# Optimization experiments

Hardware: AMD Instinct MI355X
Metric: run time of the kernel (lower is better)

Reference implementation:

```python
import jax, jax.numpy as jnp
from jax import lax
import numpy as np

B, C_IN, D, H, W = 1, 8, 48, 256, 320
BC = 8  # base_channels
DN = ('NCHW', 'OIHW', 'NCHW')


def setup_inputs() -> dict:
    key = jax.random.key(0)
    ks = iter(jax.random.split(key, 64))
    inp = {"volume_variance": jax.random.normal(next(ks), (B, C_IN, D, H, W), jnp.float32)}
    def add(name, o, i):
        inp[name + "_w"] = jax.random.normal(next(ks), (o, i, 3, 3), jnp.float32) * 0.1
        inp[name + "_b"] = jnp.zeros((o,), jnp.float32)
    add("conv1", 2 * BC, C_IN); add("conv2", 4 * BC, 2 * BC); add("conv3", 8 * BC, 4 * BC)
    add("up3", 4 * BC, 8 * BC); add("up2", 2 * BC, 4 * BC); add("up1", BC, 2 * BC)
    add("out", 1, BC)
    add("g1_gate", 2 * BC, C_IN + BC); add("g1_cand", BC, C_IN + BC)
    add("g2_gate", 4 * BC, 4 * BC); add("g2_cand", 2 * BC, 4 * BC)
    add("g3_gate", 8 * BC, 8 * BC); add("g3_cand", 4 * BC, 8 * BC)
    add("g4_gate", 16 * BC, 16 * BC); add("g4_cand", 8 * BC, 16 * BC)
    return inp


def _conv(x, w, b, stride=1):
    # Conv2d(k=3, padding=1)
    y = lax.conv_general_dilated(x, w, (stride, stride), [(1, 1), (1, 1)], dimension_numbers=DN)
    return y + b[None, :, None, None]


def _convT(x, w, b):
    # PyTorch ConvTranspose2d(k=3, s=2, p=1, output_padding=1) as an input-dilated conv
    y = lax.conv_general_dilated(x, w, (1, 1), [(1, 2), (1, 2)], lhs_dilation=(2, 2),
                                 dimension_numbers=DN)
    return y + b[None, :, None, None]


def _gru(x, h, wg, bg, wc, bc):
    # ConvGRUCell2: fused reset/update gates, tanh candidate, convex combine
    gates = jax.nn.sigmoid(_conv(jnp.concatenate([x, h], 1), wg, bg))
    r, u = jnp.split(gates, 2, 1)
    c = jnp.tanh(_conv(jnp.concatenate([x, r * h], 1), wc, bc))
    return u * h + (1.0 - u) * c


def reference(volume_variance, conv1_w, conv1_b, conv2_w, conv2_b, conv3_w, conv3_b,
              up3_w, up3_b, up2_w, up2_b, up1_w, up1_b, out_w, out_b,
              g1_gate_w, g1_gate_b, g1_cand_w, g1_cand_b,
              g2_gate_w, g2_gate_b, g2_cand_w, g2_cand_b,
              g3_gate_w, g3_gate_b, g3_cand_w, g3_cand_b,
              g4_gate_w, g4_gate_b, g4_cand_w, g4_cand_b):
    def step(carry, cost):
        s1, s2, s3, s4 = carry
        nc = -cost                                            # [B, C_IN, H, W]
        c1 = jax.nn.relu(_conv(nc, conv1_w, conv1_b, 2))      # [B, 2BC, H/2, W/2]
        c2 = jax.nn.relu(_conv(c1, conv2_w, conv2_b, 2))      # [B, 4BC, H/4, W/4]
        c3 = jax.nn.relu(_conv(c2, conv3_w, conv3_b, 2))      # [B, 8BC, H/8, W/8]
        r4 = _gru(c3, s4, g4_gate_w, g4_gate_b, g4_cand_w, g4_cand_b)
        u3 = jax.nn.relu(_convT(r4, up3_w, up3_b))            # [B, 4BC, H/4, W/4]
        r3 = _gru(c2, s3, g3_gate_w, g3_gate_b, g3_cand_w, g3_cand_b)
        u2 = jax.nn.relu(_convT(u3 + r3, up2_w, up2_b))       # [B, 2BC, H/2, W/2]
        r2 = _gru(c1, s2, g2_gate_w, g2_gate_b, g2_cand_w, g2_cand_b)
        u1 = jax.nn.relu(_convT(u2 + r2, up1_w, up1_b))       # [B, BC, H, W]
        r1 = _gru(nc, s1, g1_gate_w, g1_gate_b, g1_cand_w, g1_cand_b)
        # ConvTranspose2d(k=3, s=1, p=1, op=0) is exactly a 3x3 same-pad conv (reparam'd weight)
        reg = _conv(u1 + r1, out_w, out_b)                    # [B, 1, H, W]
        return (r1, r2, r3, r4), reg[:, 0]
    costs = jnp.moveaxis(volume_variance, 2, 0)               # [D, B, C_IN, H, W]
    init = (jnp.zeros((B, BC, H, W), jnp.float32),
            jnp.zeros((B, 2 * BC, H // 2, W // 2), jnp.float32),
            jnp.zeros((B, 4 * BC, H // 4, W // 4), jnp.float32),
            jnp.zeros((B, 8 * BC, H // 8, W // 8), jnp.float32))
    _, outs = lax.scan(step, init, costs)                     # outs: [D, B, H, W]
    return jnp.moveaxis(outs, 0, 1)                           # [B, D, H, W]
```

## Files before the change

### kernel.cpp

```cpp
#include <hip/hip_runtime.h>
#include <math.h>

namespace {

constexpr int H0 = 256, W0 = 320, H1 = 128, W1 = 160, H2 = 64, W2 = 80, H3 = 32, W3 = 40;
constexpr int HW0 = H0 * W0, HW1 = H1 * W1, HW2 = H2 * W2, HW3 = H3 * W3;
constexpr int DEPTH = 48;
constexpr int NCS = DEPTH * HW0;

__device__ __forceinline__ int xcd_remap(int b, int n) {
  const int q = n >> 3, r = n & 7, xcd = b & 7, i = b >> 3;
  return (xcd < r ? xcd * (q + 1) : r * (q + 1) + (xcd - r) * q) + i;
}

template <int CX, int CH, int COUT, int QX, int QY, int OCPT, int CHUNK,
          bool NEGX, bool CAND, int ZC, bool UNIF>
__device__ __forceinline__ void gru_conv_q(
    int bx, int by, int zg, int H, int W,
    const float* __restrict__ x, int xcs,
    const float* __restrict__ h, const float* __restrict__ rg,
    const float* __restrict__ wT, const float* __restrict__ bias,
    float* __restrict__ out, float* lds) {
  constexpr int CIN = CX + CH, TPX = 2 * QX, TPY = 2 * QY;
  constexpr int IW = TPX + 2, IH = TPY + 2;
  constexpr int NQ = QX * QY, SUBS = 256 / NQ;
  static_assert(SUBS * OCPT * ZC == COUT, "cfg");
  static_assert(CHUNK * IH * IW <= 6400, "lds");
  const int x0 = bx * TPX, y0 = by * TPY, HW = H * W, tid = threadIdx.x;
  const int q = tid % NQ, sub = tid / NQ;
  const int qx = q % QX, qy = q / QX;
  int ocb = zg * (COUT / ZC) + sub * OCPT;
  if (UNIF) ocb = __builtin_amdgcn_readfirstlane(ocb);
  float acc[OCPT][4];
#pragma unroll
  for (int j = 0; j < OCPT; j++) {
    const float bb = bias[ocb + j];
    acc[j][0] = bb; acc[j][1] = bb; acc[j][2] = bb; acc[j][3] = bb;
  }
  for (int c0 = 0; c0 < CIN; c0 += CHUNK) {
    __syncthreads();
    for (int idx = tid; idx < CHUNK * IH * IW; idx += 256) {
      const int cc = idx / (IH * IW), rr = idx % (IH * IW), yy = rr / IW, xx = rr % IW;
      const int gy = y0 + yy - 1, gx = x0 + xx - 1, c = c0 + cc;
      float v = 0.f;
      if ((unsigned)gy < (unsigned)H && (unsigned)gx < (unsigned)W) {
        if (c < CX) {
          v = x[(size_t)c * xcs + gy * W + gx];
          if (NEGX) v = -v;
        } else {
          const int p = (c - CX) * HW + gy * W + gx;
          v = h[p];
          if (CAND) v *= rg[p];
        }
      }
      lds[idx] = v;
    }
    __syncthreads();
    for (int c = 0; c < CHUNK; c++) {
      float p[4][4];
      const float* lp = lds + (c * IH + 2 * qy) * IW + 2 * qx;
#pragma unroll
      for (int r = 0; r < 4; r++) {
        const float2 a = *(const float2*)(lp + r * IW);
        const float2 b = *(const float2*)(lp + r * IW + 2);
        p[r][0] = a.x; p[r][1] = a.y; p[r][2] = b.x; p[r][3] = b.y;
      }
#pragma unroll
      for (int j = 0; j < OCPT; j++) {
        const float* wc = wT + ((size_t)(c0 + c) * COUT + ocb + j) * 9;
#pragma unroll
        for (int ky = 0; ky < 3; ky++)
#pragma unroll
          for (int kx = 0; kx < 3; kx++) {
            const float wv = wc[ky * 3 + kx];
            acc[j][0] = fmaf(p[ky][kx],         wv, acc[j][0]);
            acc[j][1] = fmaf(p[ky][kx + 1],     wv, acc[j][1]);
            acc[j][2] = fmaf(p[ky + 1][kx],     wv, acc[j][2]);
            acc[j][3] = fmaf(p[ky + 1][kx + 1], wv, acc[j][3]);
          }
      }
    }
  }
  const int ox = x0 + 2 * qx, oy = y0 + 2 * qy;
#pragma unroll
  for (int j = 0; j < OCPT; j++) {
    const int oc = ocb + j;
#pragma unroll
    for (int py = 0; py < 2; py++)
#pragma unroll
      for (int px = 0; px < 2; px++) {
        const int opix = (oy + py) * W + ox + px;
        const float a = acc[j][py * 2 + px];
        if (!CAND) {
          out[oc * HW + opix] = 1.f / (1.f + expf(-a));
        } else {
          const float cd = tanhf(a);
          const float u = rg[(CH + oc) * HW + opix];
          const float hv = h[oc * HW + opix];
          out[oc * HW + opix] = u * hv + (1.f - u) * cd;
        }
      }
  }
}

struct GruArgs {
  const float* x;
  const float* c1; const float* c2; const float* c3;
  const float* h1; const float* h2; const float* h3; const float* h4;
  const float* g1; const float* g2; const float* g3; const float* g4;
  const float* w1; const float* b1; const float* w2; const float* b2;
  const float* w3; const float* b3; const float* w4; const float* b4;
  float* o1; float* o2; float* o3; float* o4;
};

__global__ __launch_bounds__(256) void gates_k(GruArgs a) {
  __shared__ __align__(16) float lds[6400];
  const int b = xcd_remap(blockIdx.x, 1120);
  if (b < 320) {
    gru_conv_q<8, 8, 16, 8, 8, 4, 16, true, false, 1, true>(
        b % 20, b / 20, 0, H0, W0, a.x, NCS, a.h1, nullptr, a.w1, a.b1, a.o1, lds);
  } else if (b < 640) {
    const int l = b - 320;
    gru_conv_q<16, 16, 32, 8, 8, 2, 16, false, false, 4, true>(
        l % 10, (l / 10) % 8, l / 80, H1, W1, a.c1, HW1, a.h2, nullptr, a.w2, a.b2, a.o2, lds);
  } else if (b < 960) {
    const int l = b - 640;
    gru_conv_q<32, 32, 64, 4, 4, 1, 32, false, false, 4, false>(
        l % 10, (l / 10) % 8, l / 80, H2, W2, a.c2, HW2, a.h3, nullptr, a.w3, a.b3, a.o3, lds);
  } else {
    const int l = b - 960;
    gru_conv_q<64, 64, 128, 4, 4, 1, 64, false, false, 8, false>(
        l % 5, (l / 5) % 4, l / 20, H3, W3, a.c3, HW3, a.h4, nullptr, a.w4, a.b4, a.o4, lds);
  }
}

__global__ __launch_bounds__(256) void cands_k(GruArgs a) {
  __shared__ __align__(16) float lds[6400];
  const int b = xcd_remap(blockIdx.x, 720);
  if (b < 320) {
    gru_conv_q<8, 8, 8, 8, 8, 2, 16, true, true, 1, true>(
        b % 20, b / 20, 0, H0, W0, a.x, NCS, a.h1, a.g1, a.w1, a.b1, a.o1, lds);
  } else if (b < 480) {
    const int l = b - 320;
    gru_conv_q<16, 16, 16, 8, 8, 2, 16, false, true, 2, true>(
        l % 10, (l / 10) % 8, l / 80, H1, W1, a.c1, HW1, a.h2, a.g2, a.w2, a.b2, a.o2, lds);
  } else if (b < 640) {
    const int l = b - 480;
    gru_conv_q<32, 32, 32, 4, 4, 1, 32, false, true, 2, false>(
        l % 10, (l / 10) % 8, l / 80, H2, W2, a.c2, HW2, a.h3, a.g3, a.w3, a.b3, a.o3, lds);
  } else {
    const int l = b - 640;
    gru_conv_q<64, 64, 64, 4, 4, 1, 64, false, true, 4, false>(
        l % 5, (l / 5) % 4, l / 20, H3, W3, a.c3, HW3, a.h4, a.g4, a.w4, a.b4, a.o4, lds);
  }
}

template <int CIN, int COUT, int QX, int QY, int OCPT, int CHUNK, bool NEG,
          int INH, int INW, int ONH, int ONW, bool UNIF>
__global__ __launch_bounds__(256) void enc_q_k(
    const float* __restrict__ in, int inCS, size_t inTS, int inSlots,
    const float* __restrict__ wT, const float* __restrict__ bias,
    float* __restrict__ out, size_t outTS, int outSlots, int t0, int n) {
  constexpr int TPX = 2 * QX, TPY = 2 * QY, IW = 2 * TPX + 1, IH = 2 * TPY + 1;
  constexpr int SX = ONW / TPX, SY = ONH / TPY, NQ = QX * QY, SUBS = 256 / NQ;
  static_assert(SUBS * OCPT == COUT, "cfg");
  __shared__ float lds[CHUNK * IH * IW];
  const int lb = xcd_remap(blockIdx.x, n);
  const int z = lb / (SX * SY), rr = lb % (SX * SY);
  const int bx = rr % SX, by = rr / SX, tt = t0 + z;
  const float* inp = in + (size_t)(tt % inSlots) * inTS;
  float* outp = out + (size_t)(tt % outSlots) * outTS;
  const int x0 = bx * TPX, y0 = by * TPY;
  const int ix0 = 2 * x0 - 1, iy0 = 2 * y0 - 1, tid = threadIdx.x;
  const int q = tid % NQ, sub = tid / NQ, qx = q % QX, qy = q / QX;
  int ocb = sub * OCPT;
  if (UNIF) ocb = __builtin_amdgcn_readfirstlane(ocb);
  float acc[OCPT][4];
#pragma unroll
  for (int j = 0; j < OCPT; j++) {
    const float bb = bias[ocb + j];
    acc[j][0] = bb; acc[j][1] = bb; acc[j][2] = bb; acc[j][3] = bb;
  }
  for (int c0 = 0; c0 < CIN; c0 += CHUNK) {
    __syncthreads();
    for (int idx = tid; idx < CHUNK * IH * IW; idx += 256) {
      const int cc = idx / (IH * IW), r2 = idx % (IH * IW), yy = r2 / IW, xx = r2 % IW;
      const int gy = iy0 + yy, gx = ix0 + xx;
      float v = 0.f;
      if ((unsigned)gy < (unsigned)INH && (unsigned)gx < (unsigned)INW)
        v = inp[(size_t)(c0 + cc) * inCS + gy * INW + gx];
      lds[idx] = NEG ? -v : v;
    }
    __syncthreads();
    for (int c = 0; c < CHUNK; c++) {
      float p[5][5];
      const float* lp = lds + (c * IH + 4 * qy) * IW + 4 * qx;
#pragma unroll
      for (int r = 0; r < 5; r++)
#pragma unroll
        for (int s = 0; s < 5; s++) p[r][s] = lp[r * IW + s];
#pragma unroll
      for (int j = 0; j < OCPT; j++) {
        const float* wc = wT + ((size_t)(c0 + c) * COUT + ocb + j) * 9;
#pragma unroll
        for (int ky = 0; ky < 3; ky++)
#pragma unroll
          for (int kx = 0; kx < 3; kx++) {
            const float wv = wc[ky * 3 + kx];
            acc[j][0] = fmaf(p[ky][kx],         wv, acc[j][0]);
            acc[j][1] = fmaf(p[ky][kx + 2],     wv, acc[j][1]);
            acc[j][2] = fmaf(p[ky + 2][kx],     wv, acc[j][2]);
            acc[j][3] = fmaf(p[ky + 2][kx + 2], wv, acc[j][3]);
          }
      }
    }
  }
  const int ox = x0 + 2 * qx, oy = y0 + 2 * qy;
#pragma unroll
  for (int j = 0; j < OCPT; j++)
#pragma unroll
    for (int py = 0; py < 2; py++)
#pragma unroll
      for (int px = 0; px < 2; px++)
        outp[((size_t)(ocb + j) * ONH + oy + py) * ONW + ox + px] =
            fmaxf(acc[j][py * 2 + px], 0.f);
}

template <int CIN, int COUT, int OCPT, bool SUM2, int INH, int INW>
__global__ __launch_bounds__(256) void convT_q_k(
    const float* __restrict__ A, size_t aTS, int aSlots,
    const float* __restrict__ B, size_t bTS, int bSlots,
    const float* __restrict__ wT, const float* __restrict__ bias,
    float* __restrict__ out, size_t oTS, int oSlots, int t0, int n) {
  constexpr int SX = (2 * INW) / 16, SY = (2 * INH) / 16, SUBS = 16;
  static_assert(SUBS * OCPT == COUT, "cfg");
  __shared__ float lds[CIN * 81];
  const int lb = xcd_remap(blockIdx.x, n);
  const int z = lb / (SX * SY), rr = lb % (SX * SY);
  const int bx = rr % SX, by = rr / SX, tt = t0 + z;
  const float* Ap = A + (size_t)(tt % aSlots) * aTS;
  const float* Bp = B + (size_t)(tt % bSlots) * bTS;
  float* outp = out + (size_t)(tt % oSlots) * oTS;
  const int x0 = bx * 16, y0 = by * 16, ix0 = x0 / 2, iy0 = y0 / 2;
  const int HWin = INH * INW, tid = threadIdx.x;
  for (int idx = tid; idx < CIN * 81; idx += 256) {
    const int c = idx / 81, r = idx % 81, yy = r / 9, xx = r % 9;
    const int gy = iy0 + yy, gx = ix0 + xx;
    float v = 0.f;
    if (gy < INH && gx < INW) {
      const int p = c * HWin + gy * INW + gx;
      v = Ap[p];
      if (SUM2) v += Bp[p];
    }
    lds[idx] = v;
  }
  __syncthreads();
  const int cb = tid % 16, sub = tid / 16;
  const int cbx = cb % 4, cby = cb / 4;
  const int ocb = sub * OCPT;
  float a00[OCPT][4], a01[OCPT][4], a10[OCPT][4], a11[OCPT][4];
#pragma unroll
  for (int j = 0; j < OCPT; j++) {
    const float bb = bias[ocb + j];
#pragma unroll
    for (int qi = 0; qi < 4; qi++) {
      a00[j][qi] = bb; a01[j][qi] = bb; a10[j][qi] = bb; a11[j][qi] = bb;
    }
  }
  for (int c = 0; c < CIN; c++) {
    float p[3][3];
    const float* ip = lds + c * 81 + (2 * cby) * 9 + 2 * cbx;
#pragma unroll
    for (int r = 0; r < 3; r++)
#pragma unroll
      for (int s = 0; s < 3; s++) p[r][s] = ip[r * 9 + s];
#pragma unroll
    for (int j = 0; j < OCPT; j++) {
      const float* wc = wT + ((size_t)c * COUT + ocb + j) * 9;
      const float w0 = wc[0], w1 = wc[1], w2 = wc[2], w3 = wc[3], w4 = wc[4];
      const float w5 = wc[5], w6 = wc[6], w7 = wc[7], w8 = wc[8];
#pragma unroll
      for (int dy = 0; dy < 2; dy++)
#pragma unroll
        for (int dx = 0; dx < 2; dx++) {
          const int qi = dy * 2 + dx;
          const float v00 = p[dy][dx], v01 = p[dy][dx + 1];
          const float v10 = p[dy + 1][dx], v11 = p[dy + 1][dx + 1];
          a00[j][qi] = fmaf(w4, v00, a00[j][qi]);
          a01[j][qi] = fmaf(w3, v00, a01[j][qi]);
          a01[j][qi] = fmaf(w5, v01, a01[j][qi]);
          a10[j][qi] = fmaf(w1, v00, a10[j][qi]);
          a10[j][qi] = fmaf(w7, v10, a10[j][qi]);
          a11[j][qi] = fmaf(w0, v00, a11[j][qi]);
          a11[j][qi] = fmaf(w2, v01, a11[j][qi]);
          a11[j][qi] = fmaf(w6, v10, a11[j][qi]);
          a11[j][qi] = fmaf(w8, v11, a11[j][qi]);
        }
    }
  }
  const int outW = 2 * INW;
#pragma unroll
  for (int j = 0; j < OCPT; j++) {
    float* op = outp + (size_t)(ocb + j) * (4 * HWin);
#pragma unroll
    for (int dy = 0; dy < 2; dy++)
#pragma unroll
      for (int dx = 0; dx < 2; dx++) {
        const int qi = dy * 2 + dx;
        const int ox = x0 + 2 * (2 * cbx + dx), oy = y0 + 2 * (2 * cby + dy);
        const int base = oy * outW + ox;
        op[base] = fmaxf(a00[j][qi], 0.f);
        op[base + 1] = fmaxf(a01[j][qi], 0.f);
        op[base + outW] = fmaxf(a10[j][qi], 0.f);
        op[base + outW + 1] = fmaxf(a11[j][qi], 0.f);
      }
  }
}

__global__ __launch_bounds__(256) void up1out_k(
    const float* __restrict__ u2, size_t u2TS, int u2S,
    const float* __restrict__ r2, size_t r2TS, int r2S,
    const float* __restrict__ r1, size_t r1TS, int r1S,
    const float* __restrict__ wTu1, const float* __restrict__ bT,
    const float* __restrict__ wo, const float* __restrict__ bo,
    float* __restrict__ dout, int t0, int n) {
  __shared__ float ins[16 * 121];
  __shared__ float u1h[8 * 400];
  const int lb = xcd_remap(blockIdx.x, n);
  const int z = lb / 320, rr = lb % 320, bx = rr % 20, by = rr / 20;
  const int t = t0 + z;
  const float* U = u2 + (size_t)(t % u2S) * u2TS;
  const float* R2 = r2 + (size_t)(t % r2S) * r2TS;
  const float* R1 = r1 + (size_t)(t % r1S) * r1TS;
  const int x0 = bx * 16, y0 = by * 16;
  const int ix0 = x0 / 2 - 1, iy0 = y0 / 2 - 1, tid = threadIdx.x;
  for (int idx = tid; idx < 16 * 121; idx += 256) {
    const int c = idx / 121, r = idx % 121, yy = r / 11, xx = r % 11;
    const int gy = iy0 + yy, gx = ix0 + xx;
    float v = 0.f;
    if ((unsigned)gy < (unsigned)H1 && (unsigned)gx < (unsigned)W1) {
      const int p = c * HW1 + gy * W1 + gx;
      v = U[p] + R2[p];
    }
    ins[idx] = v;
  }
  __syncthreads();
  if (tid < 200) {
    const int ch = tid / 25, cb = tid % 25, cbx = cb % 5, cby = cb / 5;
    const float bb = bT[ch];
    float A0[4], A1[4], A2[4], A3[4];
#pragma unroll
    for (int qi = 0; qi < 4; qi++) { A0[qi] = bb; A1[qi] = bb; A2[qi] = bb; A3[qi] = bb; }
    for (int ic = 0; ic < 16; ic++) {
      float p[3][3];
      const float* ip = ins + ic * 121 + (2 * cby) * 11 + 2 * cbx;
#pragma unroll
      for (int r = 0; r < 3; r++)
#pragma unroll
        for (int s = 0; s < 3; s++) p[r][s] = ip[r * 11 + s];
      const float* wc = wTu1 + ((size_t)ic * 8 + ch) * 9;
      const float w0 = wc[0], w1 = wc[1], w2 = wc[2], w3 = wc[3], w4 = wc[4];
      const float w5 = wc[5], w6 = wc[6], w7 = wc[7], w8 = wc[8];
#pragma unroll
      for (int dy = 0; dy < 2; dy++)
#pragma unroll
        for (int dx = 0; dx < 2; dx++) {
          const int qi = dy * 2 + dx;
          const float v00 = p[dy][dx], v01 = p[dy][dx + 1];
          const float v10 = p[dy + 1][dx], v11 = p[dy + 1][dx + 1];
          A0[qi] = fmaf(w4, v00, A0[qi]);
          A1[qi] = fmaf(w3, v00, A1[qi]); A1[qi] = fmaf(w5, v01, A1[qi]);
          A2[qi] = fmaf(w1, v00, A2[qi]); A2[qi] = fmaf(w7, v10, A2[qi]);
          A3[qi] = fmaf(w0, v00, A3[qi]); A3[qi] = fmaf(w2, v01, A3[qi]);
          A3[qi] = fmaf(w6, v10, A3[qi]); A3[qi] = fmaf(w8, v11, A3[qi]);
        }
    }
#pragma unroll
    for (int dy = 0; dy < 2; dy++)
#pragma unroll
      for (int dx = 0; dx < 2; dx++) {
        const int qi = dy * 2 + dx;
        float* up = u1h + ch * 400 + (2 * (2 * cby + dy)) * 20 + 2 * (2 * cbx + dx);
        up[0] = fmaxf(A0[qi], 0.f);
        up[1] = fmaxf(A1[qi], 0.f);
        up[20] = fmaxf(A2[qi], 0.f);
        up[21] = fmaxf(A3[qi], 0.f);
      }
  }
  __syncthreads();
  for (int idx = tid; idx < 8 * 400; idx += 256) {
    const int c = idx / 400, r = idx % 400, hy = r / 20, hx = r % 20;
    const int gy = y0 - 2 + hy, gx = x0 - 2 + hx;
    if ((unsigned)gy < (unsigned)H0 && (unsigned)gx < (unsigned)W0)
      u1h[idx] += R1[c * HW0 + gy * W0 + gx];
    else
      u1h[idx] = 0.f;
  }
  __syncthreads();
  const int tx = tid % 16, ty = tid / 16;
  float acc = bo[0];
  for (int c = 0; c < 8; c++) {
    const float* up = u1h + c * 400 + (ty + 1) * 20 + tx + 1;
#pragma unroll
    for (int ky = 0; ky < 3; ky++)
#pragma unroll
      for (int kx = 0; kx < 3; kx++)
        acc = fmaf(up[ky * 20 + kx], wo[c * 9 + ky * 3 + kx], acc);
  }
  dout[(size_t)t * HW0 + (y0 + ty) * W0 + x0 + tx] = acc;
}

struct WT { const float* s; float* d; int O; int I; };
struct WTab { WT t[14]; };
__global__ __launch_bounds__(256) void wtrans_k(WTab a) {
  for (int ti = 0; ti < 14; ti++) {
    const int O = a.t[ti].O, I = a.t[ti].I, nn = O * I * 9;
    for (int idx = blockIdx.x * 256 + threadIdx.x; idx < nn; idx += gridDim.x * 256) {
      const int k = idx % 9, oi = idx / 9;
      const int i = oi % I, o = oi / I;
      a.t[ti].d[((size_t)i * O + o) * 9 + k] = a.t[ti].s[idx];
    }
  }
}

}

extern "C" void kernel_launch(void* const* d_in, const int* in_sizes, int n_in,
                              void* d_out, int out_size, void* d_ws, size_t ws_size,
                              hipStream_t stream) {
  const float* vol = (const float*)d_in[0];
  const float* c1w = (const float*)d_in[1];  const float* c1b = (const float*)d_in[2];
  const float* c2w = (const float*)d_in[3];  const float* c2b = (const float*)d_in[4];
  const float* c3w = (const float*)d_in[5];  const float* c3b = (const float*)d_in[6];
  const float* u3w = (const float*)d_in[7];  const float* u3b = (const float*)d_in[8];
  const float* u2w = (const float*)d_in[9];  const float* u2b = (const float*)d_in[10];
  const float* u1w = (const float*)d_in[11]; const float* u1b = (const float*)d_in[12];
  const float* ow  = (const float*)d_in[13]; const float* ob  = (const float*)d_in[14];
  const float* g1gw = (const float*)d_in[15]; const float* g1gb = (const float*)d_in[16];
  const float* g1cw = (const float*)d_in[17]; const float* g1cb = (const float*)d_in[18];
  const float* g2gw = (const float*)d_in[19]; const float* g2gb = (const float*)d_in[20];
  const float* g2cw = (const float*)d_in[21]; const float* g2cb = (const float*)d_in[22];
  const float* g3gw = (const float*)d_in[23]; const float* g3gb = (const float*)d_in[24];
  const float* g3cw = (const float*)d_in[25]; const float* g3cb = (const float*)d_in[26];
  const float* g4gw = (const float*)d_in[27]; const float* g4gb = (const float*)d_in[28];
  const float* g4cw = (const float*)d_in[29]; const float* g4cb = (const float*)d_in[30];
  float* dout = (float*)d_out;
  (void)in_sizes; (void)n_in; (void)out_size;

  const size_t r1Sz = 8 * HW0, r2Sz = 16 * HW1, r3Sz = 32 * HW2, r4Sz = 64 * HW3;
  const size_t c1Sz = 16 * HW1, c2Sz = 32 * HW2, c3Sz = 64 * HW3;
  const size_t g1Sz = 16 * HW0, g2Sz = 32 * HW1, g3Sz = 64 * HW2, g4Sz = 128 * HW3;
  const size_t ZB = 8 * HW0;
  const size_t rTot = r1Sz + r2Sz + r3Sz + r4Sz;
  const size_t cTot = c1Sz + c2Sz + c3Sz;
  const size_t gTot = g1Sz + g2Sz + g3Sz + g4Sz;
  const size_t uTot = 32 * HW2 + 16 * HW1;
  const size_t wTot = 342144;
  const size_t needA = (wTot + ZB + 48 * rTot + 48 * cTot + gTot) * sizeof(float);
  const size_t needB = (wTot + ZB + 2 * rTot + 48 * cTot + gTot + uTot) * sizeof(float);
  const int tier = ws_size >= needA ? 0 : (ws_size >= needB ? 1 : 2);
  const int TR = (tier == 0) ? 48 : 2;
  const int TC = (tier == 2) ? 1 : 48;

  float* ws = (float*)d_ws;
  size_t off = 0;
  auto alloc = [&](size_t nn) { float* p = ws + off; off += nn; return p; };
  float* wt_c1 = alloc(1152);   float* wt_c2 = alloc(4608);  float* wt_c3 = alloc(18432);
  float* wt_u3 = alloc(18432);  float* wt_u2 = alloc(4608);  float* wt_u1 = alloc(1152);
  float* wt_g1g = alloc(2304);  float* wt_g1c = alloc(1152);
  float* wt_g2g = alloc(9216);  float* wt_g2c = alloc(4608);
  float* wt_g3g = alloc(36864); float* wt_g3c = alloc(18432);
  float* wt_g4g = alloc(147456); float* wt_g4c = alloc(73728);
  float* zb = alloc(ZB);
  float* r1 = alloc((size_t)TR * r1Sz); float* r2 = alloc((size_t)TR * r2Sz);
  float* r3 = alloc((size_t)TR * r3Sz); float* r4 = alloc((size_t)TR * r4Sz);
  float* g1 = alloc(g1Sz); float* g2 = alloc(g2Sz);
  float* g3 = alloc(g3Sz); float* g4 = alloc(g4Sz);
  float* c1a = alloc((size_t)TC * c1Sz);
  float* c2a = alloc((size_t)TC * c2Sz);
  float* c3a = alloc((size_t)TC * c3Sz);
  float *u3a, *u2a;
  if (tier == 0) {
    u3a = c1a;
    u2a = c1a + 48 * (32 * HW2);
  } else {
    u3a = alloc(32 * HW2);
    u2a = alloc(16 * HW1);
  }

  WTab wt{{{c1w, wt_c1, 16, 8},   {c2w, wt_c2, 32, 16},  {c3w, wt_c3, 64, 32},
           {u3w, wt_u3, 32, 64},  {u2w, wt_u2, 16, 32},  {u1w, wt_u1, 8, 16},
           {g1gw, wt_g1g, 16, 16}, {g1cw, wt_g1c, 8, 16},
           {g2gw, wt_g2g, 32, 32}, {g2cw, wt_g2c, 16, 32},
           {g3gw, wt_g3g, 64, 64}, {g3cw, wt_g3c, 32, 64},
           {g4gw, wt_g4g, 128, 128}, {g4cw, wt_g4c, 64, 128}}};
  wtrans_k<<<dim3(128), 256, 0, stream>>>(wt);
  hipMemsetAsync(zb, 0, ZB * sizeof(float), stream);

  if (tier < 2) {
    enc_q_k<8, 16, 8, 8, 4, 8, true, 256, 320, 128, 160, true>
        <<<dim3(3840), 256, 0, stream>>>(vol, NCS, (size_t)HW0, 48, wt_c1, c1b,
                                         c1a, c1Sz, 48, 0, 3840);
    enc_q_k<16, 32, 8, 8, 8, 8, false, 128, 160, 64, 80, true>
        <<<dim3(960), 256, 0, stream>>>(c1a, HW1, c1Sz, 48, wt_c2, c2b,
                                        c2a, c2Sz, 48, 0, 960);
    enc_q_k<32, 64, 4, 4, 4, 16, false, 64, 80, 32, 40, false>
        <<<dim3(960), 256, 0, stream>>>(c2a, HW2, c2Sz, 48, wt_c3, c3b,
                                        c3a, c3Sz, 48, 0, 960);
  }

  for (int t = 0; t < DEPTH; t++) {
    if (tier == 2) {
      enc_q_k<8, 16, 8, 8, 4, 8, true, 256, 320, 128, 160, true>
          <<<dim3(80), 256, 0, stream>>>(vol, NCS, (size_t)HW0, 48, wt_c1, c1b,
                                         c1a, c1Sz, 1, t, 80);
      enc_q_k<16, 32, 8, 8, 8, 8, false, 128, 160, 64, 80, true>
          <<<dim3(20), 256, 0, stream>>>(c1a, HW1, c1Sz, 1, wt_c2, c2b,
                                         c2a, c2Sz, 1, t, 20);
      enc_q_k<32, 64, 4, 4, 4, 16, false, 64, 80, 32, 40, false>
          <<<dim3(20), 256, 0, stream>>>(c2a, HW2, c2Sz, 1, wt_c3, c3b,
                                         c3a, c3Sz, 1, t, 20);
    }
    const float* x0p = vol + (size_t)t * HW0;
    const float* h1p = t ? r1 + (size_t)((t - 1) % TR) * r1Sz : zb;
    const float* h2p = t ? r2 + (size_t)((t - 1) % TR) * r2Sz : zb;
    const float* h3p = t ? r3 + (size_t)((t - 1) % TR) * r3Sz : zb;
    const float* h4p = t ? r4 + (size_t)((t - 1) % TR) * r4Sz : zb;
    const float* c1p = c1a + (size_t)(t % TC) * c1Sz;
    const float* c2p = c2a + (size_t)(t % TC) * c2Sz;
    const float* c3p = c3a + (size_t)(t % TC) * c3Sz;
    float* o1p = r1 + (size_t)(t % TR) * r1Sz;
    float* o2p = r2 + (size_t)(t % TR) * r2Sz;
    float* o3p = r3 + (size_t)(t % TR) * r3Sz;
    float* o4p = r4 + (size_t)(t % TR) * r4Sz;

    GruArgs ga{x0p, c1p, c2p, c3p, h1p, h2p, h3p, h4p,
               nullptr, nullptr, nullptr, nullptr,
               wt_g1g, g1gb, wt_g2g, g2gb, wt_g3g, g3gb, wt_g4g, g4gb,
               g1, g2, g3, g4};
    gates_k<<<dim3(1120), 256, 0, stream>>>(ga);
    GruArgs ca{x0p, c1p, c2p, c3p, h1p, h2p, h3p, h4p,
               g1, g2, g3, g4,
               wt_g1c, g1cb, wt_g2c, g2cb, wt_g3c, g3cb, wt_g4c, g4cb,
               o1p, o2p, o3p, o4p};
    cands_k<<<dim3(720), 256, 0, stream>>>(ca);

    if (tier > 0) {
      convT_q_k<64, 32, 2, false, 32, 40>
          <<<dim3(20), 256, 0, stream>>>(r4, r4Sz, TR, r4, 0, 1, wt_u3, u3b,
                                         u3a, (size_t)32 * HW2, 1, t, 20);
      convT_q_k<32, 16, 1, true, 64, 80>
          <<<dim3(80), 256, 0, stream>>>(u3a, (size_t)32 * HW2, 1, r3, r3Sz, TR,
                                         wt_u2, u2b, u2a, (size_t)16 * HW1, 1, t, 80);
      up1out_k<<<dim3(320), 256, 0, stream>>>(
          u2a, (size_t)16 * HW1, 1, r2, r2Sz, TR, r1, r1Sz, TR,
          wt_u1, u1b, ow, ob, dout, t, 320);
    }
  }

  if (tier == 0) {
    convT_q_k<64, 32, 2, false, 32, 40>
        <<<dim3(960), 256, 0, stream>>>(r4, r4Sz, 48, r4, 0, 1, wt_u3, u3b,
                                        u3a, (size_t)32 * HW2, 48, 0, 960);
    convT_q_k<32, 16, 1, true, 64, 80>
        <<<dim3(3840), 256, 0, stream>>>(u3a, (size_t)32 * HW2, 48, r3, r3Sz, 48,
                                         wt_u2, u2b, u2a, (size_t)16 * HW1, 48, 0, 3840);
    up1out_k<<<dim3(15360), 256, 0, stream>>>(
        u2a, (size_t)16 * HW1, 48, r2, r2Sz, 48, r1, r1Sz, 48,
        wt_u1, u1b, ow, ob, dout, 0, 15360);
  }
}
```

Measured before the change: 9.838 ms.

## Restructure GRU conv tiling to one pixel per thread with wave-uniform channels

Replaces the 2x2-quad-per-thread GRU conv with a one-output-pixel-per-thread scheme. The level-1 path uses 16x16 tiles with all output channels per thread, and the coarser levels use 8x8 tiles with a per-wave channel group read via readfirstlane. Multi-chunk levels precompute packed gather offsets once and load larger channel chunks into LDS. Launch bounds now request 5 blocks per CU, grids are rebalanced, and the final up1out launch in tier 0 is split into four smaller launches. Together this trades quad-level input reuse for scalar weight broadcasts and higher occupancy, with more register pressure from the wide per-thread channel accumulators.

```diff
diff --git a/kernel.cpp b/kernel.cpp
--- a/kernel.cpp
+++ b/kernel.cpp
@@ -13,42 +13,58 @@
   return (xcd < r ? xcd * (q + 1) : r * (q + 1) + (xcd - r) * q) + i;
 }
 
-template <int CX, int CH, int COUT, int QX, int QY, int OCPT, int CHUNK,
-          bool NEGX, bool CAND, int ZC, bool UNIF>
-__device__ __forceinline__ void gru_conv_q(
+template <int CX, int CH, int COUT, int TW, int TH, int OCW, int CHUNK,
+          bool AMODE, bool NEGX, bool CAND>
+__device__ __forceinline__ void gru5(
     int bx, int by, int zg, int H, int W,
     const float* __restrict__ x, int xcs,
     const float* __restrict__ h, const float* __restrict__ rg,
     const float* __restrict__ wT, const float* __restrict__ bias,
     float* __restrict__ out, float* lds) {
-  constexpr int CIN = CX + CH, TPX = 2 * QX, TPY = 2 * QY;
-  constexpr int IW = TPX + 2, IH = TPY + 2;
-  constexpr int NQ = QX * QY, SUBS = 256 / NQ;
-  static_assert(SUBS * OCPT * ZC == COUT, "cfg");
-  static_assert(CHUNK * IH * IW <= 6400, "lds");
-  const int x0 = bx * TPX, y0 = by * TPY, HW = H * W, tid = threadIdx.x;
-  const int q = tid % NQ, sub = tid / NQ;
-  const int qx = q % QX, qy = q / QX;
-  int ocb = zg * (COUT / ZC) + sub * OCPT;
-  if (UNIF) ocb = __builtin_amdgcn_readfirstlane(ocb);
-  float acc[OCPT][4];
-#pragma unroll
-  for (int j = 0; j < OCPT; j++) {
-    const float bb = bias[ocb + j];
-    acc[j][0] = bb; acc[j][1] = bb; acc[j][2] = bb; acc[j][3] = bb;
-  }
-  for (int c0 = 0; c0 < CIN; c0 += CHUNK) {
-    __syncthreads();
-    for (int idx = tid; idx < CHUNK * IH * IW; idx += 256) {
-      const int cc = idx / (IH * IW), rr = idx % (IH * IW), yy = rr / IW, xx = rr % IW;
-      const int gy = y0 + yy - 1, gx = x0 + xx - 1, c = c0 + cc;
+  constexpr int CIN = CX + CH, IW = TW + 2, IH = TH + 2, NST = IH * IW;
+  constexpr int NCHK = CIN / CHUNK, TOTAL = CHUNK * NST;
+  static_assert(NCHK * CHUNK == CIN, "chunk");
+  static_assert(AMODE ? (TW == 16 && TH == 16) : (TW == 8 && TH == 8), "tile");
+  const int tid = threadIdx.x, wv = tid >> 6, ln = tid & 63;
+  const int x0 = bx * TW, y0 = by * TH, HW = H * W;
+  int lx, ly, ocb;
+  if (AMODE) {
+    lx = ln & 15; ly = (wv << 2) + (ln >> 4); ocb = 0;
+  } else {
+    lx = ln & 7; ly = ln >> 3;
+    ocb = __builtin_amdgcn_readfirstlane((zg * 4 + wv) * OCW);
+  }
+  float acc[OCW];
+#pragma unroll
+  for (int j = 0; j < OCW; j++) acc[j] = bias[ocb + j];
+
+  auto compute = [&](int c0) {
+    for (int c = 0; c < CHUNK; c++) {
+      float v[9];
+      const float* lp = lds + (c * IH + ly) * IW + lx;
+#pragma unroll
+      for (int ky = 0; ky < 3; ky++)
+#pragma unroll
+        for (int kx = 0; kx < 3; kx++) v[ky * 3 + kx] = lp[ky * IW + kx];
+      const float* wb = wT + ((size_t)(c0 + c) * COUT + ocb) * 9;
+#pragma unroll
+      for (int j = 0; j < OCW; j++)
+#pragma unroll
+        for (int k = 0; k < 9; k++) acc[j] = fmaf(v[k], wb[j * 9 + k], acc[j]);
+    }
+  };
+
+  if constexpr (NCHK == 1) {
+    for (int idx = tid; idx < TOTAL; idx += 256) {
+      const int cc = idx / NST, rr = idx % NST, yy = rr / IW, xx = rr % IW;
+      const int gy = y0 + yy - 1, gx = x0 + xx - 1;
       float v = 0.f;
       if ((unsigned)gy < (unsigned)H && (unsigned)gx < (unsigned)W) {
-        if (c < CX) {
-          v = x[(size_t)c * xcs + gy * W + gx];
+        if (cc < CX) {
+          v = x[(size_t)cc * xcs + gy * W + gx];
           if (NEGX) v = -v;
         } else {
-          const int p = (c - CX) * HW + gy * W + gx;
+          const int p = (cc - CX) * HW + gy * W + gx;
           v = h[p];
           if (CAND) v *= rg[p];
         }
@@ -56,50 +72,57 @@
       lds[idx] = v;
     }
     __syncthreads();
-    for (int c = 0; c < CHUNK; c++) {
-      float p[4][4];
-      const float* lp = lds + (c * IH + 2 * qy) * IW + 2 * qx;
-#pragma unroll
-      for (int r = 0; r < 4; r++) {
-        const float2 a = *(const float2*)(lp + r * IW);
-        const float2 b = *(const float2*)(lp + r * IW + 2);
-        p[r][0] = a.x; p[r][1] = a.y; p[r][2] = b.x; p[r][3] = b.y;
+    compute(0);
+  } else {
+    constexpr int NIT = TOTAL / 256;
+    static_assert(NIT * 256 == TOTAL, "items");
+    unsigned pk[NIT];
+#pragma unroll
+    for (int i = 0; i < NIT; i++) {
+      const int idx = tid + 256 * i;
+      const int cc = idx / NST, rr = idx % NST, yy = rr / IW, xx = rr % IW;
+      const int gy = y0 + yy - 1, gx = x0 + xx - 1;
+      const bool val = (unsigned)gy < (unsigned)H && (unsigned)gx < (unsigned)W;
+      const unsigned ro = val ? (unsigned)(gy * W + gx) : 0u;
+      pk[i] = (val ? 0x80000000u : 0u) | ((unsigned)cc << 20) | ro;
+    }
+    for (int c0 = 0; c0 < CIN; c0 += CHUNK) {
+      if (c0) __syncthreads();
+#pragma unroll
+      for (int i = 0; i < NIT; i++) {
+        const unsigned u = pk[i];
+        float v = 0.f;
+        if (u & 0x80000000u) {
+          const int c = c0 + (int)((u >> 20) & 0x3ffu);
+          const int ro = (int)(u & 0xfffffu);
+          if (c < CX) {
+            v = x[(size_t)c * xcs + ro];
+            if (NEGX) v = -v;
+          } else {
+            const int p = (c - CX) * HW + ro;
+            v = h[p];
+            if (CAND) v *= rg[p];
+          }
+        }
+        lds[tid + 256 * i] = v;
       }
-#pragma unroll
-      for (int j = 0; j < OCPT; j++) {
-        const float* wc = wT + ((size_t)(c0 + c) * COUT + ocb + j) * 9;
-#pragma unroll
-        for (int ky = 0; ky < 3; ky++)
-#pragma unroll
-          for (int kx = 0; kx < 3; kx++) {
-            const float wv = wc[ky * 3 + kx];
-            acc[j][0] = fmaf(p[ky][kx],         wv, acc[j][0]);
-            acc[j][1] = fmaf(p[ky][kx + 1],     wv, acc[j][1]);
-            acc[j][2] = fmaf(p[ky + 1][kx],     wv, acc[j][2]);
-            acc[j][3] = fmaf(p[ky + 1][kx + 1], wv, acc[j][3]);
-          }
-      }
-    }
-  }
-  const int ox = x0 + 2 * qx, oy = y0 + 2 * qy;
-#pragma unroll
-  for (int j = 0; j < OCPT; j++) {
+      __syncthreads();
+      compute(c0);
+    }
+  }
+
+  const int opix = (y0 + ly) * W + x0 + lx;
+#pragma unroll
+  for (int j = 0; j < OCW; j++) {
     const int oc = ocb + j;
-#pragma unroll
-    for (int py = 0; py < 2; py++)
-#pragma unroll
-      for (int px = 0; px < 2; px++) {
-        const int opix = (oy + py) * W + ox + px;
-        const float a = acc[j][py * 2 + px];
-        if (!CAND) {
-          out[oc * HW + opix] = 1.f / (1.f + expf(-a));
-        } else {
-          const float cd = tanhf(a);
-          const float u = rg[(CH + oc) * HW + opix];
-          const float hv = h[oc * HW + opix];
-          out[oc * HW + opix] = u * hv + (1.f - u) * cd;
-        }
-      }
+    if (!CAND) {
+      out[oc * HW + opix] = 1.f / (1.f + expf(-acc[j]));
+    } else {
+      const float cd = tanhf(acc[j]);
+      const float u = rg[(CH + oc) * HW + opix];
+      const float hv = h[oc * HW + opix];
+      out[oc * HW + opix] = u * hv + (1.f - u) * cd;
+    }
   }
 }
 
@@ -113,45 +136,45 @@
   float* o1; float* o2; float* o3; float* o4;
 };
 
-__global__ __launch_bounds__(256) void gates_k(GruArgs a) {
+__global__ __launch_bounds__(256, 5) void gates_k(GruArgs a) {
   __shared__ __align__(16) float lds[6400];
-  const int b = xcd_remap(blockIdx.x, 1120);
+  const int b = xcd_remap(blockIdx.x, 1280);
   if (b < 320) {
-    gru_conv_q<8, 8, 16, 8, 8, 4, 16, true, false, 1, true>(
+    gru5<8, 8, 16, 16, 16, 16, 16, true, true, false>(
         b % 20, b / 20, 0, H0, W0, a.x, NCS, a.h1, nullptr, a.w1, a.b1, a.o1, lds);
   } else if (b < 640) {
     const int l = b - 320;
-    gru_conv_q<16, 16, 32, 8, 8, 2, 16, false, false, 4, true>(
-        l % 10, (l / 10) % 8, l / 80, H1, W1, a.c1, HW1, a.h2, nullptr, a.w2, a.b2, a.o2, lds);
+    gru5<16, 16, 32, 8, 8, 8, 32, false, false, false>(
+        l % 20, l / 20, 0, H1, W1, a.c1, HW1, a.h2, nullptr, a.w2, a.b2, a.o2, lds);
   } else if (b < 960) {
-    const int l = b - 640;
-    gru_conv_q<32, 32, 64, 4, 4, 1, 32, false, false, 4, false>(
-        l % 10, (l / 10) % 8, l / 80, H2, W2, a.c2, HW2, a.h3, nullptr, a.w3, a.b3, a.o3, lds);
+    const int l = b - 640, t = l >> 2, zg = l & 3;
+    gru5<32, 32, 64, 8, 8, 4, 64, false, false, false>(
+        t % 10, t / 10, zg, H2, W2, a.c2, HW2, a.h3, nullptr, a.w3, a.b3, a.o3, lds);
   } else {
-    const int l = b - 960;
-    gru_conv_q<64, 64, 128, 4, 4, 1, 64, false, false, 8, false>(
-        l % 5, (l / 5) % 4, l / 20, H3, W3, a.c3, HW3, a.h4, nullptr, a.w4, a.b4, a.o4, lds);
-  }
-}
-
-__global__ __launch_bounds__(256) void cands_k(GruArgs a) {
+    const int l = b - 960, t = l >> 4, zg = l & 15;
+    gru5<64, 64, 128, 8, 8, 2, 64, false, false, false>(
+        t % 5, t / 5, zg, H3, W3, a.c3, HW3, a.h4, nullptr, a.w4, a.b4, a.o4, lds);
+  }
+}
+
+__global__ __launch_bounds__(256, 5) void cands_k(GruArgs a) {
   __shared__ __align__(16) float lds[6400];
-  const int b = xcd_remap(blockIdx.x, 720);
+  const int b = xcd_remap(blockIdx.x, 1280);
   if (b < 320) {
-    gru_conv_q<8, 8, 8, 8, 8, 2, 16, true, true, 1, true>(
+    gru5<8, 8, 8, 16, 16, 8, 16, true, true, true>(
         b % 20, b / 20, 0, H0, W0, a.x, NCS, a.h1, a.g1, a.w1, a.b1, a.o1, lds);
-  } else if (b < 480) {
+  } else if (b < 640) {
     const int l = b - 320;
-    gru_conv_q<16, 16, 16, 8, 8, 2, 16, false, true, 2, true>(
-        l % 10, (l / 10) % 8, l / 80, H1, W1, a.c1, HW1, a.h2, a.g2, a.w2, a.b2, a.o2, lds);
-  } else if (b < 640) {
-    const int l = b - 480;
-    gru_conv_q<32, 32, 32, 4, 4, 1, 32, false, true, 2, false>(
-        l % 10, (l / 10) % 8, l / 80, H2, W2, a.c2, HW2, a.h3, a.g3, a.w3, a.b3, a.o3, lds);
+    gru5<16, 16, 16, 8, 8, 4, 32, false, false, true>(
+        l % 20, l / 20, 0, H1, W1, a.c1, HW1, a.h2, a.g2, a.w2, a.b2, a.o2, lds);
+  } else if (b < 960) {
+    const int l = b - 640, t = l >> 2, zg = l & 3;
+    gru5<32, 32, 32, 8, 8, 2, 64, false, false, true>(
+        t % 10, t / 10, zg, H2, W2, a.c2, HW2, a.h3, a.g3, a.w3, a.b3, a.o3, lds);
   } else {
-    const int l = b - 640;
-    gru_conv_q<64, 64, 64, 4, 4, 1, 64, false, true, 4, false>(
-        l % 5, (l / 5) % 4, l / 20, H3, W3, a.c3, HW3, a.h4, a.g4, a.w4, a.b4, a.o4, lds);
+    const int l = b - 960, t = l >> 4, zg = l & 15;
+    gru5<64, 64, 64, 8, 8, 1, 64, false, false, true>(
+        t % 5, t / 5, zg, H3, W3, a.c3, HW3, a.h4, a.g4, a.w4, a.b4, a.o4, lds);
   }
 }
 
@@ -538,12 +561,12 @@
                nullptr, nullptr, nullptr, nullptr,
                wt_g1g, g1gb, wt_g2g, g2gb, wt_g3g, g3gb, wt_g4g, g4gb,
                g1, g2, g3, g4};
-    gates_k<<<dim3(1120), 256, 0, stream>>>(ga);
+    gates_k<<<dim3(1280), 256, 0, stream>>>(ga);
     GruArgs ca{x0p, c1p, c2p, c3p, h1p, h2p, h3p, h4p,
                g1, g2, g3, g4,
                wt_g1c, g1cb, wt_g2c, g2cb, wt_g3c, g3cb, wt_g4c, g4cb,
                o1p, o2p, o3p, o4p};
-    cands_k<<<dim3(720), 256, 0, stream>>>(ca);
+    cands_k<<<dim3(1280), 256, 0, stream>>>(ca);
 
     if (tier > 0) {
       convT_q_k<64, 32, 2, false, 32, 40>
@@ -565,8 +588,9 @@
     convT_q_k<32, 16, 1, true, 64, 80>
         <<<dim3(3840), 256, 0, stream>>>(u3a, (size_t)32 * HW2, 48, r3, r3Sz, 48,
                                          wt_u2, u2b, u2a, (size_t)16 * HW1, 48, 0, 3840);
-    up1out_k<<<dim3(15360), 256, 0, stream>>>(
-        u2a, (size_t)16 * HW1, 48, r2, r2Sz, 48, r1, r1Sz, 48,
-        wt_u1, u1b, ow, ob, dout, 0, 15360);
-  }
-}
+    for (int tc = 0; tc < 4; tc++)
+      up1out_k<<<dim3(3840), 256, 0, stream>>>(
+          u2a, (size_t)16 * HW1, 48, r2, r2Sz, 48, r1, r1Sz, 48,
+          wt_u1, u1b, ow, ob, dout, 12 * tc, 3840);
+  }
+}
```

Measured after the change: 10.13 ms. +3.0%, slower.
